# Performance work log

Measured on AMD Instinct MI355X. Metric: run time of the kernel, lower is better.

The kernel has to match this reference:

```python
import jax, jax.numpy as jnp
import numpy as np

DEPTH = 4  # truncation depth of the signature


def setup_inputs() -> dict:
    key = jax.random.key(0)
    # path: (batch, stream, channels)
    path = jax.random.normal(key, (128, 128, 12), dtype=jnp.float32)
    return {"path": path}


def _exp_terms(d, depth):
    """Tensor exponential of a single linear increment d: (B, C).

    Returns a tuple of flattened levels; level k has shape (B, C**k) and
    equals d^{\otimes k} / k!.
    """
    B = d.shape[0]
    terms = [d]
    for k in range(2, depth + 1):
        terms.append(jnp.einsum('bi,bj->bij', terms[-1], d).reshape(B, -1) / k)
    return tuple(terms)


def _signature(path, depth):
    """Truncated path signature (stream=False, basepoint=False).

    Combines per-increment tensor exponentials with Chen's identity:
    (A \otimes B)_m = A_m + B_m + sum_{i=1}^{m-1} A_i \otimes B_{m-i}.
    """
    B, L, C = path.shape
    dx = path[:, 1:] - path[:, :-1]  # (B, L-1, C) path increments
    init = _exp_terms(dx[:, 0], depth)

    def step(sig, d):
        e = _exp_terms(d, depth)
        new = []
        for m in range(1, depth + 1):  # signature level m, shape (B, C**m)
            t = sig[m - 1] + e[m - 1]
            for i in range(1, m):  # cross terms sig_i (x) e_{m-i}
                t = t + jnp.einsum('bi,bj->bij', sig[i - 1], e[m - i - 1]).reshape(B, -1)
            new.append(t)
        return tuple(new), None

    # scan over the remaining L-2 increments (time-major)
    sig, _ = jax.lax.scan(step, init, jnp.transpose(dx[:, 1:], (1, 0, 2)))
    # flatten levels in order 1..depth, matching signatory's layout
    return jnp.concatenate(sig, axis=-1)  # (B, C + C^2 + ... + C^depth)


def reference(path):
    return _signature(path, DEPTH)
```

## Files before the change

kernel.cpp:

```cpp
#include <hip/hip_runtime.h>


#define NC    12
#define NPTS  128
#define NSTEP 128
#define OUT_PER_B 22620
#define B1 384
#define B2 448
#define PADQ 33

typedef float vf16 __attribute__((ext_vector_type(16)));

#define WGET(e) ((e) < 16 ? w0[(e) & 15] : ((e) < 32 ? w1[(e) & 15] : w2[(e) & 15]))

__global__ __launch_bounds__(B1)
void prep_kernel(const float* __restrict__ path, float* __restrict__ Draw,
                 float* __restrict__ DTg) {
    const int b = blockIdx.x;
    const int t = threadIdx.x;
    const int c  = t >> 5;
    const int sq = t & 31;
    const float* pb = path + (size_t)b * (NPTS * NC);
    float d[4];
    #pragma unroll
    for (int e = 0; e < 4; ++e) {
        int s = 4 * sq + e;
        d[e] = (s < NPTS - 1) ? (pb[(s + 1) * NC + c] - pb[s * NC + c]) : 0.f;
        Draw[(size_t)b * 1536 + s * NC + c] = d[e];
    }
    float4* dtg = (float4*)(DTg + (size_t)b * 1536 + c * NSTEP);
    dtg[sq] = make_float4(d[0], d[1], d[2], d[3]);
}

__global__ __launch_bounds__(B2)
void sig_kernel(const float* __restrict__ Draw, const float* __restrict__ DTg,
                float* __restrict__ out) {
    const int bid = blockIdx.x;
    const int b  = bid >> 1;
    const int ih = bid & 1;
    const int t  = threadIdx.x;

    __shared__ __align__(16) float4 DT4[NC * PADQ];

    if (t < NC * 32) {
        int c = t >> 5, sq = t & 31;
        const float4* src = (const float4*)(DTg + (size_t)b * 1536 + c * NSTEP);
        DT4[c * PADQ + sq] = src[sq];
    }
    __syncthreads();

    const int ta  = (t < 432) ? t : (t - 432);
    const int il  = ta / 72;
    const int rem = ta - il * 72;
    const int j   = rem / 6;
    const int kh  = rem - j * 6;
    const int i   = ih * 6 + il;
    const int k0  = kh * 2;

    float acc0[12], acc1[12];
    #pragma unroll
    for (int l = 0; l < 12; ++l) { acc0[l] = 0.f; acc1[l] = 0.f; }
    float s3a = 0.f, s3b = 0.f, s2 = 0.f, s1 = 0.f;

    unsigned long long base_u;
    {
        unsigned long long a = (unsigned long long)(Draw + (size_t)b * 1536);
        unsigned int lo = __builtin_amdgcn_readfirstlane((unsigned int)a);
        unsigned int hi = __builtin_amdgcn_readfirstlane((unsigned int)(a >> 32));
        base_u = ((unsigned long long)hi << 32) | lo;
    }

    const float4* dti  = &DT4[i * PADQ];
    const float4* dtj  = &DT4[j * PADQ];
    const float4* dtka = &DT4[k0 * PADQ];
    const float4* dtkb = &DT4[(k0 + 1) * PADQ];

    for (int sq = 0; sq < NSTEP / 4; ++sq) {
        vf16 w0, w1, w2;
        {
            const float* wp = (const float*)(base_u + (unsigned long long)(sq * 192));
            asm volatile(
                "s_load_dwordx16 %0, %3, 0x0\n\t"
                "s_load_dwordx16 %1, %3, 0x40\n\t"
                "s_load_dwordx16 %2, %3, 0x80\n\t"
                "s_waitcnt lgkmcnt(0)"
                : "=&s"(w0), "=&s"(w1), "=&s"(w2)
                : "s"(wp));
        }

        float4 di4  = dti[sq];
        float4 dj4  = dtj[sq];
        float4 dka4 = dtka[sq];
        float4 dkb4 = dtkb[sq];

        #pragma unroll
        for (int u = 0; u < 4; ++u) {
            const float di  = (&di4.x)[u];
            const float dj  = (&dj4.x)[u];
            const float dka = (&dka4.x)[u];
            const float dkb = (&dkb4.x)[u];

            float A4  = (s1 + 0.25f * di) * (1.f / 3.f);
            float B4  = (s2 + dj * A4) * 0.5f;
            float C3a = s3a + dka * B4;
            float C3b = s3b + dkb * B4;

            #pragma unroll
            for (int l = 0; l < 12; ++l) {
                const float wl = WGET(12 * u + l);
                acc0[l] += C3a * wl;
                acc1[l] += C3b * wl;
            }

            float A3 = (s1 + di * (1.f / 3.f)) * 0.5f;
            float C2 = s2 + dj * A3;
            s3a += dka * C2;
            s3b += dkb * C2;
            s2  += dj * (s1 + 0.5f * di);
            s1  += di;
        }
    }

    if (t < 432) {
        float* ob = out + (size_t)b * OUT_PER_B;
        if (j == 0 && kh == 0) ob[i] = s1;
        if (kh == 0) ob[12 + i * 12 + j] = s2;
        const int ijk = (i * 12 + j) * 12 + k0;
        ob[156 + ijk]     = s3a;
        ob[156 + ijk + 1] = s3b;
        float4* o4 = (float4*)(ob + 1884 + (size_t)ijk * 12);
        o4[0] = make_float4(acc0[0], acc0[1], acc0[2],  acc0[3]);
        o4[1] = make_float4(acc0[4], acc0[5], acc0[6],  acc0[7]);
        o4[2] = make_float4(acc0[8], acc0[9], acc0[10], acc0[11]);
        o4[3] = make_float4(acc1[0], acc1[1], acc1[2],  acc1[3]);
        o4[4] = make_float4(acc1[4], acc1[5], acc1[6],  acc1[7]);
        o4[5] = make_float4(acc1[8], acc1[9], acc1[10], acc1[11]);
    }
}

extern "C" void kernel_launch(void* const* d_in, const int* in_sizes, int n_in,
                              void* d_out, int out_size, void* d_ws, size_t ws_size,
                              hipStream_t stream) {
    const float* path = (const float*)d_in[0];
    float* out = (float*)d_out;
    const int nbatch = in_sizes[0] / (NPTS * NC);

    float* Draw = (float*)d_ws;
    float* DTg  = Draw + (size_t)nbatch * 1536;

    prep_kernel<<<nbatch, B1, 0, stream>>>(path, Draw, DTg);
    sig_kernel<<<nbatch * 2, B2, 0, stream>>>(Draw, DTg, out);
}
```

Baseline: 79.33 us.

## Fuse increment prep into signature kernel and read weights from LDS

Removes the separate prep kernel: each block loads its batch's path into shared memory, computes the increments there and builds both the row-major weight array and the transposed padded layout. The inner loop now reads per-step increment vectors from LDS as broadcast float4 loads instead of scalar s_load from global memory. This saves one kernel launch and the global round-trip through the workspace, at the cost of each of the two blocks per batch redoing the diff and using more LDS and VGPRs for the weight vectors.

After: 73.47 us, median of 2. -7.4%, faster.

```diff
diff --git a/kernel.cpp b/kernel.cpp
--- a/kernel.cpp
+++ b/kernel.cpp
@@ -5,47 +5,35 @@
 #define NPTS  128
 #define NSTEP 128
 #define OUT_PER_B 22620
-#define B1 384
-#define B2 448
+#define BT 448
 #define PADQ 33
 
-typedef float vf16 __attribute__((ext_vector_type(16)));
-
-#define WGET(e) ((e) < 16 ? w0[(e) & 15] : ((e) < 32 ? w1[(e) & 15] : w2[(e) & 15]))
-
-__global__ __launch_bounds__(B1)
-void prep_kernel(const float* __restrict__ path, float* __restrict__ Draw,
-                 float* __restrict__ DTg) {
-    const int b = blockIdx.x;
-    const int t = threadIdx.x;
-    const int c  = t >> 5;
-    const int sq = t & 31;
-    const float* pb = path + (size_t)b * (NPTS * NC);
-    float d[4];
-    #pragma unroll
-    for (int e = 0; e < 4; ++e) {
-        int s = 4 * sq + e;
-        d[e] = (s < NPTS - 1) ? (pb[(s + 1) * NC + c] - pb[s * NC + c]) : 0.f;
-        Draw[(size_t)b * 1536 + s * NC + c] = d[e];
-    }
-    float4* dtg = (float4*)(DTg + (size_t)b * 1536 + c * NSTEP);
-    dtg[sq] = make_float4(d[0], d[1], d[2], d[3]);
-}
-
-__global__ __launch_bounds__(B2)
-void sig_kernel(const float* __restrict__ Draw, const float* __restrict__ DTg,
-                float* __restrict__ out) {
+__global__ __launch_bounds__(BT)
+void sig_kernel(const float* __restrict__ path, float* __restrict__ out) {
     const int bid = blockIdx.x;
     const int b  = bid >> 1;
     const int ih = bid & 1;
     const int t  = threadIdx.x;
 
+    __shared__ __align__(16) float  P[NPTS * NC];
+    __shared__ __align__(16) float  W[NSTEP * NC];
     __shared__ __align__(16) float4 DT4[NC * PADQ];
 
-    if (t < NC * 32) {
-        int c = t >> 5, sq = t & 31;
-        const float4* src = (const float4*)(DTg + (size_t)b * 1536 + c * NSTEP);
-        DT4[c * PADQ + sq] = src[sq];
+    const float* pb = path + (size_t)b * (NPTS * NC);
+    if (t < 384) ((float4*)P)[t] = ((const float4*)pb)[t];
+    __syncthreads();
+
+    if (t < 384) {
+        const int c  = t >> 5;
+        const int sq = t & 31;
+        float d[4];
+        #pragma unroll
+        for (int e = 0; e < 4; ++e) {
+            const int s = 4 * sq + e;
+            d[e] = (s < NPTS - 1) ? (P[(s + 1) * NC + c] - P[s * NC + c]) : 0.f;
+            W[s * NC + c] = d[e];
+        }
+        DT4[c * PADQ + sq] = make_float4(d[0], d[1], d[2], d[3]);
     }
     __syncthreads();
 
@@ -62,31 +50,16 @@
     for (int l = 0; l < 12; ++l) { acc0[l] = 0.f; acc1[l] = 0.f; }
     float s3a = 0.f, s3b = 0.f, s2 = 0.f, s1 = 0.f;
 
-    unsigned long long base_u;
-    {
-        unsigned long long a = (unsigned long long)(Draw + (size_t)b * 1536);
-        unsigned int lo = __builtin_amdgcn_readfirstlane((unsigned int)a);
-        unsigned int hi = __builtin_amdgcn_readfirstlane((unsigned int)(a >> 32));
-        base_u = ((unsigned long long)hi << 32) | lo;
-    }
-
+    const float4* wt   = (const float4*)W;
     const float4* dti  = &DT4[i * PADQ];
     const float4* dtj  = &DT4[j * PADQ];
     const float4* dtka = &DT4[k0 * PADQ];
     const float4* dtkb = &DT4[(k0 + 1) * PADQ];
 
     for (int sq = 0; sq < NSTEP / 4; ++sq) {
-        vf16 w0, w1, w2;
-        {
-            const float* wp = (const float*)(base_u + (unsigned long long)(sq * 192));
-            asm volatile(
-                "s_load_dwordx16 %0, %3, 0x0\n\t"
-                "s_load_dwordx16 %1, %3, 0x40\n\t"
-                "s_load_dwordx16 %2, %3, 0x80\n\t"
-                "s_waitcnt lgkmcnt(0)"
-                : "=&s"(w0), "=&s"(w1), "=&s"(w2)
-                : "s"(wp));
-        }
+        float4 wq[12];
+        #pragma unroll
+        for (int q = 0; q < 12; ++q) wq[q] = wt[sq * 12 + q];
 
         float4 di4  = dti[sq];
         float4 dj4  = dtj[sq];
@@ -107,7 +80,7 @@
 
             #pragma unroll
             for (int l = 0; l < 12; ++l) {
-                const float wl = WGET(12 * u + l);
+                const float wl = (&wq[3 * u + (l >> 2)].x)[l & 3];
                 acc0[l] += C3a * wl;
                 acc1[l] += C3b * wl;
             }
@@ -145,9 +118,5 @@
     float* out = (float*)d_out;
     const int nbatch = in_sizes[0] / (NPTS * NC);
 
-    float* Draw = (float*)d_ws;
-    float* DTg  = Draw + (size_t)nbatch * 1536;
-
-    prep_kernel<<<nbatch, B1, 0, stream>>>(path, Draw, DTg);
-    sig_kernel<<<nbatch * 2, B2, 0, stream>>>(Draw, DTg, out);
+    sig_kernel<<<nbatch * 2, BT, 0, stream>>>(path, out);
 }
```
